# Performance work log

Measured on AMD Instinct MI355X. Metric: run time of the kernel, lower is better.

Reference implementation:

```python
import jax, jax.numpy as jnp
import numpy as np

EMBED = 1024
HEADS = 16
HEAD_DIM = EMBED // HEADS
HIDDEN = int(EMBED * 4.0)
EPS = 1e-6


def setup_inputs() -> dict:
    key = jax.random.key(0)
    ks = jax.random.split(key, 8)
    s = lambda fan_in: 1.0 / np.sqrt(fan_in)
    x = jax.random.normal(ks[0], (2, 2048, EMBED), dtype=jnp.float32)
    return {
        "x": x,
        "ln1_g": jnp.ones((EMBED,), jnp.float32),
        "ln1_b": jnp.zeros((EMBED,), jnp.float32),
        "w_qkv": jax.random.normal(ks[1], (EMBED, 3 * EMBED), jnp.float32) * s(EMBED),
        "b_qkv": jnp.zeros((3 * EMBED,), jnp.float32),
        "w_proj": jax.random.normal(ks[2], (EMBED, EMBED), jnp.float32) * s(EMBED),
        "b_proj": jnp.zeros((EMBED,), jnp.float32),
        "ln2_g": jnp.ones((EMBED,), jnp.float32),
        "ln2_b": jnp.zeros((EMBED,), jnp.float32),
        "w_fc1": jax.random.normal(ks[3], (EMBED, HIDDEN), jnp.float32) * s(EMBED),
        "b_fc1": jnp.zeros((HIDDEN,), jnp.float32),
        "w_fc2": jax.random.normal(ks[4], (HIDDEN, EMBED), jnp.float32) * s(HIDDEN),
        "b_fc2": jnp.zeros((EMBED,), jnp.float32),
    }


def _layernorm(x, g, b):
    mu = jnp.mean(x, axis=-1, keepdims=True)
    var = jnp.mean(jnp.square(x - mu), axis=-1, keepdims=True)
    return (x - mu) * jax.lax.rsqrt(var + EPS) * g + b


def _attention(x, w_qkv, b_qkv, w_proj, b_proj):
    B, N, C = x.shape
    qkv = x @ w_qkv + b_qkv                      # [B,N,3C]
    qkv = qkv.reshape(B, N, 3, HEADS, HEAD_DIM)
    q, k, v = (qkv[:, :, 0], qkv[:, :, 1], qkv[:, :, 2])  # [B,N,H,Dh]
    scale = HEAD_DIM ** -0.5
    attn = jnp.einsum('bnhd,bmhd->bhnm', q, k) * scale     # [B,H,N,N]
    attn = jax.nn.softmax(attn, axis=-1)
    out = jnp.einsum('bhnm,bmhd->bnhd', attn, v).reshape(B, N, C)
    return out @ w_proj + b_proj


def reference(x, ln1_g, ln1_b, w_qkv, b_qkv, w_proj, b_proj,
              ln2_g, ln2_b, w_fc1, b_fc1, w_fc2, b_fc2):
    x = x + _attention(_layernorm(x, ln1_g, ln1_b), w_qkv, b_qkv, w_proj, b_proj)
    h = _layernorm(x, ln2_g, ln2_b)
    h = jax.nn.gelu(h @ w_fc1 + b_fc1, approximate=False)
    x = x + (h @ w_fc2 + b_fc2)
    return x
```

## Files before the change

### kernel.cpp

```cpp
#include <hip/hip_runtime.h>
#include <hip/hip_bf16.h>
#include <math.h>

typedef __bf16 bf16x8 __attribute__((ext_vector_type(8)));
typedef __bf16 bf16x4 __attribute__((ext_vector_type(4)));
typedef unsigned short u16x8 __attribute__((ext_vector_type(8)));
typedef float f32x4 __attribute__((ext_vector_type(4)));

#define EP_QKV 0
#define EP_GELU 1
#define EP_RES 2

static __device__ __forceinline__ unsigned short f2bf(float x) {
  unsigned int u = __float_as_uint(x);
  unsigned int r = (u + 0x7fffu + ((u >> 16) & 1u)) >> 16;
  return (unsigned short)r;
}

static __device__ __forceinline__ unsigned int pkbf(float lo, float hi) {
  return __builtin_amdgcn_perm(__float_as_uint(hi), __float_as_uint(lo), 0x07060302);
}

static __device__ __forceinline__ void async16(const void* g, void* l) {
  __builtin_amdgcn_global_load_lds((__attribute__((address_space(1))) void*)g,
                                   (__attribute__((address_space(3))) void*)l, 16, 0, 0);
}

__global__ __launch_bounds__(256) void wt_transpose(const float* __restrict__ in,
                                                    unsigned short* __restrict__ out,
                                                    int K, int N) {
  __shared__ float tile[32][33];
  const int n0 = blockIdx.x * 32;
  const int k0 = blockIdx.y * 32;
  const int tx = threadIdx.x;
  const int ty = threadIdx.y;
  #pragma unroll
  for (int i = ty; i < 32; i += 8)
    tile[i][tx] = in[(size_t)(k0 + i) * N + n0 + tx];
  __syncthreads();
  #pragma unroll
  for (int i = ty; i < 32; i += 8)
    out[(size_t)(n0 + i) * K + k0 + tx] = f2bf(tile[tx][i]);
}

__global__ __launch_bounds__(256) void ln_kernel(const float* __restrict__ x,
                                                 const float* __restrict__ g,
                                                 const float* __restrict__ b,
                                                 unsigned short* __restrict__ outp) {
  const int row = blockIdx.x;
  const int tid = threadIdx.x;
  const int wave = tid >> 6, lane = tid & 63;
  const float4 v = ((const float4*)(x + (size_t)row * 1024))[tid];
  float s = v.x + v.y + v.z + v.w;
  #pragma unroll
  for (int i = 1; i < 64; i <<= 1) s += __shfl_xor(s, i);
  __shared__ float red[4];
  if (lane == 0) red[wave] = s;
  __syncthreads();
  const float mean = (red[0] + red[1] + red[2] + red[3]) * (1.f / 1024.f);
  const float dx = v.x - mean, dy = v.y - mean, dz = v.z - mean, dw = v.w - mean;
  float ss = dx * dx + dy * dy + dz * dz + dw * dw;
  #pragma unroll
  for (int i = 1; i < 64; i <<= 1) ss += __shfl_xor(ss, i);
  __syncthreads();
  if (lane == 0) red[wave] = ss;
  __syncthreads();
  const float var = (red[0] + red[1] + red[2] + red[3]) * (1.f / 1024.f);
  const float inv = rsqrtf(var + 1e-6f);
  const float4 gv = ((const float4*)g)[tid];
  const float4 bv = ((const float4*)b)[tid];
  ushort4 o;
  o.x = f2bf(dx * inv * gv.x + bv.x);
  o.y = f2bf(dy * inv * gv.y + bv.y);
  o.z = f2bf(dz * inv * gv.z + bv.z);
  o.w = f2bf(dw * inv * gv.w + bv.w);
  ((ushort4*)(outp + (size_t)row * 1024))[tid] = o;
}

template <int TN, int BK>
__global__ __launch_bounds__(256) void gemm_kernel(
    const unsigned short* __restrict__ A,
    const unsigned short* __restrict__ BT,
    const float* __restrict__ bias,
    int M, int N, int K, int mode,
    void* __restrict__ outp, const float* __restrict__ res) {
  constexpr int AM = (TN == 128) ? 4 : 2;
  constexpr int ACH = BK / 16;
  constexpr int BCH = TN * BK / 2048;
  constexpr int CPR = BK / 8;
  constexpr int ABYTES = 256 * BK;
  constexpr int BBYTES = TN * BK * 2;
  __shared__ __align__(16) char smem[2 * (ABYTES + BBYTES)];

  const int tid = threadIdx.x;
  const int wave = tid >> 6, lane = tid & 63;
  const int quad = lane >> 4, l16 = lane & 15;
  const int wm = (TN == 128) ? (wave >> 1) : wave;
  const int wn = (TN == 128) ? (wave & 1) : 0;

  const int nbm = M >> 7, nbn = N / TN;
  const int lin = blockIdx.y * gridDim.x + blockIdx.x;
  const int g = lin & 7, idx = lin >> 3;
  const int gm = nbm >> 2, gn = nbn >> 1;
  const int bm = (g & 3) * gm + (idx % gm);
  const int bn = (g >> 2) * gn + (idx / gm);
  const int row_m = bm * 128, row_n = bn * TN;

  int ar[ACH], ac[ACH];
  #pragma unroll
  for (int i = 0; i < ACH; ++i) {
    const int c = wave * (64 * ACH) + i * 64 + lane;
    ar[i] = c / CPR;
    ac[i] = ((c % CPR) ^ (ar[i] & (CPR - 1))) * 8;
  }
  int br[BCH], bc[BCH];
  #pragma unroll
  for (int i = 0; i < BCH; ++i) {
    const int c = wave * (64 * BCH) + i * 64 + lane;
    br[i] = c / CPR;
    bc[i] = ((c % CPR) ^ (br[i] & (CPR - 1))) * 8;
  }

  const unsigned short* Ag = A + (size_t)row_m * K;
  const unsigned short* Bg = BT + (size_t)row_n * K;

  const f32x4 z = {0.f, 0.f, 0.f, 0.f};
  f32x4 acc[AM][4];
  #pragma unroll
  for (int i = 0; i < AM; ++i)
    #pragma unroll
    for (int j = 0; j < 4; ++j) acc[i][j] = z;

  auto issue = [&](int kt, int b) {
    unsigned short* As = (unsigned short*)(smem + b * ABYTES);
    unsigned short* Bs = (unsigned short*)(smem + 2 * ABYTES + b * BBYTES);
    #pragma unroll
    for (int i = 0; i < ACH; ++i)
      async16(Ag + (size_t)ar[i] * K + kt + ac[i], As + wave * (ACH * 512) + i * 512);
    #pragma unroll
    for (int i = 0; i < BCH; ++i)
      async16(Bg + (size_t)br[i] * K + kt + bc[i], Bs + wave * (BCH * 512) + i * 512);
  };

  issue(0, 0);
  for (int kt = 0; kt < K; kt += BK) {
    const int b = (kt / BK) & 1;
    __syncthreads();
    if (kt + BK < K) issue(kt + BK, b ^ 1);
    const unsigned short* As = (const unsigned short*)(smem + b * ABYTES);
    const unsigned short* Bs = (const unsigned short*)(smem + 2 * ABYTES + b * BBYTES);
    #pragma unroll
    for (int h = 0; h < BK / 32; ++h) {
      bf16x8 af[AM], bfv[4];
      #pragma unroll
      for (int t = 0; t < AM; ++t) {
        const int row = wm * (AM * 16) + t * 16 + l16;
        const int ch = (h * 4 + quad) ^ (row & (CPR - 1));
        af[t] = *(const bf16x8*)(As + row * BK + ch * 8);
      }
      #pragma unroll
      for (int t = 0; t < 4; ++t) {
        const int row = wn * 64 + t * 16 + l16;
        const int ch = (h * 4 + quad) ^ (row & (CPR - 1));
        bfv[t] = *(const bf16x8*)(Bs + row * BK + ch * 8);
      }
      #pragma unroll
      for (int tm = 0; tm < AM; ++tm)
        #pragma unroll
        for (int tn = 0; tn < 4; ++tn)
          acc[tm][tn] = __builtin_amdgcn_mfma_f32_16x16x32_bf16(af[tm], bfv[tn], acc[tm][tn], 0, 0, 0);
    }
  }

  #pragma unroll
  for (int tn = 0; tn < 4; ++tn) {
    const int col = row_n + wn * 64 + tn * 16 + l16;
    const float bv = bias[col];
    #pragma unroll
    for (int tm = 0; tm < AM; ++tm) {
      const int rbase = row_m + wm * (AM * 16) + tm * 16 + quad * 4;
      float v[4];
      #pragma unroll
      for (int r = 0; r < 4; ++r) v[r] = acc[tm][tn][r] + bv;
      if (mode == EP_QKV) {
        unsigned short* outw = (unsigned short*)outp;
        const int which = col >> 10;
        const int h = (col >> 6) & 15, d = col & 63;
        const int bb = rbase >> 11, n = rbase & 2047;
        const size_t bh = (size_t)(bb * 16 + h);
        if (which == 0) {
          #pragma unroll
          for (int r = 0; r < 4; ++r)
            outw[(bh * 2048 + n + r) * 64 + d] = f2bf(v[r] * 0.18033688011112043f);
        } else if (which == 1) {
          #pragma unroll
          for (int r = 0; r < 4; ++r)
            outw[4194304ull + (bh * 2048 + n + r) * 64 + d] = f2bf(v[r]);
        } else {
          uint2 o;
          o.x = pkbf(v[0], v[1]);
          o.y = pkbf(v[2], v[3]);
          *(uint2*)(outw + 8388608ull + (bh * 64 + d) * 2048 + n) = o;
        }
      } else if (mode == EP_GELU) {
        #pragma unroll
        for (int r = 0; r < 4; ++r) {
          const float u = v[r];
          const float c = 1.5957691216f * fmaf(0.044715f * u * u, u, u);
          const float e = __expf(c);
          const float gl = u - __fdividef(u, e + 1.0f);
          ((unsigned short*)outp)[(size_t)(rbase + r) * N + col] = f2bf(gl);
        }
      } else {
        #pragma unroll
        for (int r = 0; r < 4; ++r)
          ((float*)outp)[(size_t)(rbase + r) * N + col] =
              res[(size_t)(rbase + r) * N + col] + v[r];
      }
    }
  }
}

__global__ __launch_bounds__(256, 3) void attn_kernel(
    const unsigned short* __restrict__ Q,
    const unsigned short* __restrict__ Kb,
    const unsigned short* __restrict__ VT,
    unsigned short* __restrict__ outp) {
  __shared__ __align__(16) char smem[49152];
  unsigned short* Ks = (unsigned short*)smem;
  unsigned short* Vs = (unsigned short*)(smem + 32768);

  const int tid = threadIdx.x;
  const int wave = tid >> 6, lane = tid & 63;
  const int quad = lane >> 4, l16 = lane & 15;

  const int lin = blockIdx.y * gridDim.x + blockIdx.x;
  const int g = lin & 7, idx = lin >> 3;
  const int bhi = g * 4 + (idx >> 5);
  const int q0 = (idx & 31) * 64;

  const unsigned short* Qg = Q + ((size_t)bhi * 2048 + q0) * 64;
  const unsigned short* Kg = Kb + (size_t)bhi * 2048 * 64;
  const unsigned short* Vg = VT + (size_t)bhi * 64 * 2048;

  const unsigned short* kp[4];
  const unsigned short* vp[4];
  #pragma unroll
  for (int i = 0; i < 4; ++i) {
    const int c = wave * 256 + i * 64 + lane;
    const int krr = c >> 3, kcc = ((c & 7) ^ (krr & 7)) * 8;
    const int vrr = c >> 4, vcc = ((c & 15) ^ (vrr & 15)) * 8;
    kp[i] = Kg + (size_t)krr * 64 + kcc;
    vp[i] = Vg + (size_t)vrr * 2048 + vcc;
  }

  auto issueK = [&](int b) {
    unsigned short* Kd = Ks + b * 8192;
    #pragma unroll
    for (int i = 0; i < 4; ++i) async16(kp[i], Kd + wave * 2048 + i * 512);
    #pragma unroll
    for (int i = 0; i < 4; ++i) kp[i] += 8192;
  };
  auto issueV = [&]() {
    #pragma unroll
    for (int i = 0; i < 4; ++i) async16(vp[i], Vs + wave * 2048 + i * 512);
    #pragma unroll
    for (int i = 0; i < 4; ++i) vp[i] += 128;
  };

  issueK(0);

  bf16x8 qb[4][2];
  #pragma unroll
  for (int nt = 0; nt < 4; ++nt)
    #pragma unroll
    for (int h = 0; h < 2; ++h)
      qb[nt][h] = *(const bf16x8*)(Qg + (nt * 16 + l16) * 64 + (h * 4 + quad) * 8);

  const f32x4 z = {0.f, 0.f, 0.f, 0.f};
  f32x4 acc[4][4];
  #pragma unroll
  for (int i = 0; i < 4; ++i)
    #pragma unroll
    for (int j = 0; j < 4; ++j) acc[i][j] = z;
  float lsum[4] = {0.f, 0.f, 0.f, 0.f};

  const int rowA = wave * 16 + l16;
  const int rowB = 64 + rowA;
  const int swk = l16 & 7;
  const float C2 = 23.083120654223414f;

  bf16x8 pb[4];
  auto computeQK = [&](int b) {
    const unsigned short* Ksb = Ks + b * 8192;
    f32x4 sA[4], sB[4];
    #pragma unroll
    for (int nt = 0; nt < 4; ++nt) { sA[nt] = z; sB[nt] = z; }
    #pragma unroll
    for (int h = 0; h < 2; ++h) {
      const int ch = (h * 4 + quad) ^ swk;
      bf16x8 kfA = *(const bf16x8*)(Ksb + rowA * 64 + ch * 8);
      bf16x8 kfB = *(const bf16x8*)(Ksb + rowB * 64 + ch * 8);
      #pragma unroll
      for (int nt = 0; nt < 4; ++nt) {
        sA[nt] = __builtin_amdgcn_mfma_f32_16x16x32_bf16(kfA, qb[nt][h], sA[nt], 0, 0, 0);
        sB[nt] = __builtin_amdgcn_mfma_f32_16x16x32_bf16(kfB, qb[nt][h], sB[nt], 0, 0, 0);
      }
    }
    #pragma unroll
    for (int nt = 0; nt < 4; ++nt) {
      union { unsigned int d[4]; bf16x8 b; } cv;
      float pa[4], pv[4];
      float ls = 0.f;
      #pragma unroll
      for (int r = 0; r < 4; ++r) {
        pa[r] = __builtin_amdgcn_exp2f(sA[nt][r] - C2);
        pv[r] = __builtin_amdgcn_exp2f(sB[nt][r] - C2);
        ls += pa[r] + pv[r];
      }
      cv.d[0] = pkbf(pa[0], pa[1]);
      cv.d[1] = pkbf(pa[2], pa[3]);
      cv.d[2] = pkbf(pv[0], pv[1]);
      cv.d[3] = pkbf(pv[2], pv[3]);
      lsum[nt] += ls;
      pb[nt] = cv.b;
    }
  };

  auto computePV = [&]() {
    #pragma unroll
    for (int mt = 0; mt < 4; ++mt) {
      const int d = mt * 16 + l16;
      const int cA = (wave * 2 + (quad >> 1)) ^ (d & 15);
      const int cB = (8 + wave * 2 + (quad >> 1)) ^ (d & 15);
      const int sub = (quad & 1) * 4;
      bf16x4 vA = *(const bf16x4*)(Vs + d * 128 + cA * 8 + sub);
      bf16x4 vB = *(const bf16x4*)(Vs + d * 128 + cB * 8 + sub);
      bf16x8 vf = __builtin_shufflevector(vA, vB, 0, 1, 2, 3, 4, 5, 6, 7);
      #pragma unroll
      for (int nt = 0; nt < 4; ++nt)
        acc[mt][nt] = __builtin_amdgcn_mfma_f32_16x16x32_bf16(vf, pb[nt], acc[mt][nt], 0, 0, 0);
    }
  };

  for (int t = 0; t < 16; ++t) {
    __syncthreads();
    issueV();
    issueK((t + 1) & 1);
    computeQK(t & 1);
    asm volatile("s_waitcnt vmcnt(4) lgkmcnt(0)\n\ts_barrier" ::: "memory");
    computePV();
  }
  __syncthreads();

  float* sc = (float*)smem;
  float* lred = (float*)(smem + 32768);
  #pragma unroll
  for (int nt = 0; nt < 4; ++nt) {
    float ls = lsum[nt];
    ls += __shfl_xor(ls, 16);
    ls += __shfl_xor(ls, 32);
    if (quad == 0) lred[wave * 64 + nt * 16 + l16] = ls;
  }
  if (wave >= 2) {
    float* dst = sc + (wave - 2) * 4096;
    #pragma unroll
    for (int mt = 0; mt < 4; ++mt)
      #pragma unroll
      for (int nt = 0; nt < 4; ++nt)
        *(f32x4*)(dst + (mt * 4 + nt) * 256 + lane * 4) = acc[mt][nt];
  }
  __syncthreads();
  if (wave < 2) {
    const float* src = sc + wave * 4096;
    #pragma unroll
    for (int mt = 0; mt < 4; ++mt)
      #pragma unroll
      for (int nt = 0; nt < 4; ++nt)
        acc[mt][nt] += *(const f32x4*)(src + (mt * 4 + nt) * 256 + lane * 4);
  }
  if (wave == 1) {
    float* dst = sc + 4096;
    #pragma unroll
    for (int mt = 0; mt < 4; ++mt)
      #pragma unroll
      for (int nt = 0; nt < 4; ++nt)
        *(f32x4*)(dst + (mt * 4 + nt) * 256 + lane * 4) = acc[mt][nt];
  }
  __syncthreads();
  if (wave == 0) {
    const float* src = sc + 4096;
    float linv[4];
    #pragma unroll
    for (int nt = 0; nt < 4; ++nt) {
      const int qi = nt * 16 + l16;
      const float l = lred[qi] + lred[64 + qi] + lred[128 + qi] + lred[192 + qi];
      linv[nt] = 1.0f / l;
    }
    const int b = bhi >> 4, h = bhi & 15;
    #pragma unroll
    for (int mt = 0; mt < 4; ++mt)
      #pragma unroll
      for (int nt = 0; nt < 4; ++nt) {
        f32x4 o = acc[mt][nt] + *(const f32x4*)(src + (mt * 4 + nt) * 256 + lane * 4);
        uint2 ov;
        ov.x = pkbf(o[0] * linv[nt], o[1] * linv[nt]);
        ov.y = pkbf(o[2] * linv[nt], o[3] * linv[nt]);
        *(uint2*)(outp + ((size_t)(b * 2048 + q0 + nt * 16 + l16)) * 1024 +
                  h * 64 + mt * 16 + quad * 4) = ov;
      }
  }
}

extern "C" void kernel_launch(void* const* d_in, const int* in_sizes, int n_in,
                              void* d_out, int out_size, void* d_ws, size_t ws_size,
                              hipStream_t stream) {
  (void)in_sizes; (void)n_in; (void)out_size; (void)ws_size;
  const float* x      = (const float*)d_in[0];
  const float* ln1_g  = (const float*)d_in[1];
  const float* ln1_b  = (const float*)d_in[2];
  const float* w_qkv  = (const float*)d_in[3];
  const float* b_qkv  = (const float*)d_in[4];
  const float* w_proj = (const float*)d_in[5];
  const float* b_proj = (const float*)d_in[6];
  const float* ln2_g  = (const float*)d_in[7];
  const float* ln2_b  = (const float*)d_in[8];
  const float* w_fc1  = (const float*)d_in[9];
  const float* b_fc1  = (const float*)d_in[10];
  const float* w_fc2  = (const float*)d_in[11];
  const float* b_fc2  = (const float*)d_in[12];

  char* ws = (char*)d_ws;
  unsigned short* wqkvT  = (unsigned short*)(ws + 0);
  unsigned short* wprojT = (unsigned short*)(ws + 6291456);
  unsigned short* wfc1T  = (unsigned short*)(ws + 8388608);
  unsigned short* wfc2T  = (unsigned short*)(ws + 16777216);
  unsigned short* lnb    = (unsigned short*)(ws + 25165824);
  unsigned short* qkvb   = (unsigned short*)(ws + 33554432);
  unsigned short* attnb  = (unsigned short*)(ws + 58720256);
  float*          x2     = (float*)(ws + 67108864);
  unsigned short* hbuf   = qkvb;

  dim3 tb(32, 8);
  wt_transpose<<<dim3(96, 32), tb, 0, stream>>>(w_qkv, wqkvT, 1024, 3072);
  wt_transpose<<<dim3(32, 32), tb, 0, stream>>>(w_proj, wprojT, 1024, 1024);
  wt_transpose<<<dim3(128, 32), tb, 0, stream>>>(w_fc1, wfc1T, 1024, 4096);
  wt_transpose<<<dim3(32, 128), tb, 0, stream>>>(w_fc2, wfc2T, 4096, 1024);

  ln_kernel<<<4096, 256, 0, stream>>>(x, ln1_g, ln1_b, lnb);

  gemm_kernel<128, 64><<<dim3(24, 32), 256, 0, stream>>>(lnb, wqkvT, b_qkv, 4096, 3072, 1024,
                                                         EP_QKV, (void*)qkvb, nullptr);

  attn_kernel<<<dim3(32, 32), 256, 0, stream>>>(qkvb, qkvb + 4194304, qkvb + 8388608, attnb);

  gemm_kernel<64, 64><<<dim3(16, 32), 256, 0, stream>>>(attnb, wprojT, b_proj, 4096, 1024, 1024,
                                                        EP_RES, (void*)x2, x);

  ln_kernel<<<4096, 256, 0, stream>>>(x2, ln2_g, ln2_b, lnb);

  gemm_kernel<128, 64><<<dim3(32, 32), 256, 0, stream>>>(lnb, wfc1T, b_fc1, 4096, 4096, 1024,
                                                         EP_GELU, (void*)hbuf, nullptr);

  gemm_kernel<64, 64><<<dim3(16, 32), 256, 0, stream>>>(hbuf, wfc2T, b_fc2, 4096, 1024, 4096,
                                                        EP_RES, d_out, x2);
}
```

Before: 338.3 us.

## Load attention K/V fragments straight from global into registers, dropping LDS staging

```diff
diff --git a/kernel.cpp b/kernel.cpp
--- a/kernel.cpp
+++ b/kernel.cpp
@@ -221,14 +221,12 @@
   }
 }
 
-__global__ __launch_bounds__(256, 3) void attn_kernel(
+__global__ __launch_bounds__(256, 2) void attn_kernel(
     const unsigned short* __restrict__ Q,
     const unsigned short* __restrict__ Kb,
     const unsigned short* __restrict__ VT,
     unsigned short* __restrict__ outp) {
-  __shared__ __align__(16) char smem[49152];
-  unsigned short* Ks = (unsigned short*)smem;
-  unsigned short* Vs = (unsigned short*)(smem + 32768);
+  __shared__ __align__(16) char smem[33792];
 
   const int tid = threadIdx.x;
   const int wave = tid >> 6, lane = tid & 63;
@@ -243,32 +241,9 @@
   const unsigned short* Kg = Kb + (size_t)bhi * 2048 * 64;
   const unsigned short* Vg = VT + (size_t)bhi * 64 * 2048;
 
-  const unsigned short* kp[4];
-  const unsigned short* vp[4];
-  #pragma unroll
-  for (int i = 0; i < 4; ++i) {
-    const int c = wave * 256 + i * 64 + lane;
-    const int krr = c >> 3, kcc = ((c & 7) ^ (krr & 7)) * 8;
-    const int vrr = c >> 4, vcc = ((c & 15) ^ (vrr & 15)) * 8;
-    kp[i] = Kg + (size_t)krr * 64 + kcc;
-    vp[i] = Vg + (size_t)vrr * 2048 + vcc;
-  }
-
-  auto issueK = [&](int b) {
-    unsigned short* Kd = Ks + b * 8192;
-    #pragma unroll
-    for (int i = 0; i < 4; ++i) async16(kp[i], Kd + wave * 2048 + i * 512);
-    #pragma unroll
-    for (int i = 0; i < 4; ++i) kp[i] += 8192;
-  };
-  auto issueV = [&]() {
-    #pragma unroll
-    for (int i = 0; i < 4; ++i) async16(vp[i], Vs + wave * 2048 + i * 512);
-    #pragma unroll
-    for (int i = 0; i < 4; ++i) vp[i] += 128;
-  };
-
-  issueK(0);
+  const int rowA = wave * 16 + l16;
+  const int rowB = 64 + rowA;
+  const int voff = wave * 16 + (quad >> 1) * 8 + (quad & 1) * 4;
 
   bf16x8 qb[4][2];
   #pragma unroll
@@ -285,28 +260,39 @@
     for (int j = 0; j < 4; ++j) acc[i][j] = z;
   float lsum[4] = {0.f, 0.f, 0.f, 0.f};
 
-  const int rowA = wave * 16 + l16;
-  const int rowB = 64 + rowA;
-  const int swk = l16 & 7;
   const float C2 = 23.083120654223414f;
 
-  bf16x8 pb[4];
-  auto computeQK = [&](int b) {
-    const unsigned short* Ksb = Ks + b * 8192;
+  auto loadK = [&](int t, bf16x8 (&dA)[2], bf16x8 (&dB)[2]) {
+    const unsigned short* Kt = Kg + (size_t)t * 8192;
+    #pragma unroll
+    for (int h = 0; h < 2; ++h) {
+      dA[h] = *(const bf16x8*)(Kt + rowA * 64 + (h * 4 + quad) * 8);
+      dB[h] = *(const bf16x8*)(Kt + rowB * 64 + (h * 4 + quad) * 8);
+    }
+  };
+
+  auto tile = [&](int t, bf16x8 (&kA)[2], bf16x8 (&kB)[2],
+                  bf16x8 (&nA)[2], bf16x8 (&nB)[2]) {
+    const unsigned short* Vt = Vg + t * 128 + voff;
+    bf16x4 vA[4], vB[4];
+    #pragma unroll
+    for (int mt = 0; mt < 4; ++mt) {
+      const size_t o = (size_t)(mt * 16 + l16) * 2048;
+      vA[mt] = *(const bf16x4*)(Vt + o);
+      vB[mt] = *(const bf16x4*)(Vt + o + 64);
+    }
     f32x4 sA[4], sB[4];
     #pragma unroll
     for (int nt = 0; nt < 4; ++nt) { sA[nt] = z; sB[nt] = z; }
     #pragma unroll
-    for (int h = 0; h < 2; ++h) {
-      const int ch = (h * 4 + quad) ^ swk;
-      bf16x8 kfA = *(const bf16x8*)(Ksb + rowA * 64 + ch * 8);
-      bf16x8 kfB = *(const bf16x8*)(Ksb + rowB * 64 + ch * 8);
+    for (int h = 0; h < 2; ++h)
       #pragma unroll
       for (int nt = 0; nt < 4; ++nt) {
-        sA[nt] = __builtin_amdgcn_mfma_f32_16x16x32_bf16(kfA, qb[nt][h], sA[nt], 0, 0, 0);
-        sB[nt] = __builtin_amdgcn_mfma_f32_16x16x32_bf16(kfB, qb[nt][h], sB[nt], 0, 0, 0);
-      }
-    }
+        sA[nt] = __builtin_amdgcn_mfma_f32_16x16x32_bf16(kA[h], qb[nt][h], sA[nt], 0, 0, 0);
+        sB[nt] = __builtin_amdgcn_mfma_f32_16x16x32_bf16(kB[h], qb[nt][h], sB[nt], 0, 0, 0);
+      }
+    loadK(t + 1, nA, nB);
+    bf16x8 pb[4];
     #pragma unroll
     for (int nt = 0; nt < 4; ++nt) {
       union { unsigned int d[4]; bf16x8 b; } cv;
@@ -325,31 +311,20 @@
       lsum[nt] += ls;
       pb[nt] = cv.b;
     }
-  };
-
-  auto computePV = [&]() {
     #pragma unroll
     for (int mt = 0; mt < 4; ++mt) {
-      const int d = mt * 16 + l16;
-      const int cA = (wave * 2 + (quad >> 1)) ^ (d & 15);
-      const int cB = (8 + wave * 2 + (quad >> 1)) ^ (d & 15);
-      const int sub = (quad & 1) * 4;
-      bf16x4 vA = *(const bf16x4*)(Vs + d * 128 + cA * 8 + sub);
-      bf16x4 vB = *(const bf16x4*)(Vs + d * 128 + cB * 8 + sub);
-      bf16x8 vf = __builtin_shufflevector(vA, vB, 0, 1, 2, 3, 4, 5, 6, 7);
+      bf16x8 vf = __builtin_shufflevector(vA[mt], vB[mt], 0, 1, 2, 3, 4, 5, 6, 7);
       #pragma unroll
       for (int nt = 0; nt < 4; ++nt)
         acc[mt][nt] = __builtin_amdgcn_mfma_f32_16x16x32_bf16(vf, pb[nt], acc[mt][nt], 0, 0, 0);
     }
   };
 
-  for (int t = 0; t < 16; ++t) {
-    __syncthreads();
-    issueV();
-    issueK((t + 1) & 1);
-    computeQK(t & 1);
-    asm volatile("s_waitcnt vmcnt(4) lgkmcnt(0)\n\ts_barrier" ::: "memory");
-    computePV();
+  bf16x8 k0A[2], k0B[2], k1A[2], k1B[2];
+  loadK(0, k0A, k0B);
+  for (int t = 0; t < 16; t += 2) {
+    tile(t, k0A, k0B, k1A, k1B);
+    tile(t + 1, k1A, k1B, k0A, k0B);
   }
   __syncthreads();
 
```

New measurement: 370.1 us. 9.4% more time.
